# Kernel optimization log

Hardware: AMD Instinct MI355X
Metric: run time of the kernel (lower is better)

## Reference

```python
import jax, jax.numpy as jnp
import numpy as np

D_MODEL = 4096
D_FIBER = 16
D_CONTROL = 64
EMA_MOMENTUM = 0.9


def setup_inputs() -> dict:
    key = jax.random.key(0)
    k_h, k_f, k_w1, k_w2 = jax.random.split(key, 4)
    B, S = 4, 2048
    hidden = jax.random.normal(k_h, (B, S, D_MODEL), dtype=jnp.float32)
    # torch nn.Linear stores weight as [out, in]; fiber_proj init: normal std=0.02
    W_fiber = jax.random.normal(k_f, (D_FIBER, D_MODEL), dtype=jnp.float32) * 0.02
    # predictor[0]: Linear(d_model+d_fiber, d_control) with default torch init (uniform)
    fan_in1 = D_MODEL + D_FIBER
    bound1 = 1.0 / np.sqrt(fan_in1)
    W1 = jax.random.uniform(k_w1, (D_CONTROL, fan_in1), dtype=jnp.float32, minval=-bound1, maxval=bound1)
    b1 = jnp.zeros((D_CONTROL,), dtype=jnp.float32)
    # predictor[-2]: Linear(d_control, 1), weight normal std=0.01, bias zero
    W2 = jax.random.normal(k_w2, (1, D_CONTROL), dtype=jnp.float32) * 0.01
    b2 = jnp.zeros((1,), dtype=jnp.float32)
    lam = jnp.asarray(1.0, dtype=jnp.float32)
    return {"hidden": hidden, "W_fiber": W_fiber, "W1": W1, "b1": b1, "W2": W2, "b2": b2, "lam": lam}


def _causal_ema(delta_h, alpha):
    # h_t = alpha*h_{t-1} + (1-alpha)*d_t, h_{-1} = 0. delta_h: [B,S]
    B = delta_h.shape[0]
    def step(h_prev, d_t):
        h_t = alpha * h_prev + (1.0 - alpha) * d_t
        return h_t, h_t
    _, hs = jax.lax.scan(step, jnp.zeros((B,), delta_h.dtype), jnp.swapaxes(delta_h, 0, 1))
    return jnp.swapaxes(hs, 0, 1)  # [B,S]


def reference(hidden, W_fiber, W1, b1, W2, b2, lam):
    h = hidden.astype(jnp.float32)                      # [B,S,D]
    fiber = jnp.einsum('bsd,fd->bsf', h, W_fiber)       # [B,S,16]
    combined = jnp.concatenate([h, fiber], axis=-1)     # [B,S,D+16]
    z = jax.nn.gelu(jnp.einsum('bsc,kc->bsk', combined, W1) + b1, approximate=False)
    delta_h = jax.nn.softplus(jnp.einsum('bsk,ok->bso', z, W2) + b2)[..., 0]  # [B,S]
    field = _causal_ema(delta_h, EMA_MOMENTUM)          # [B,S]
    gate = jax.nn.sigmoid(-lam * field)
    return gate.astype(hidden.dtype), field.astype(hidden.dtype), delta_h.mean()
```

## Files before the change

### kernel.cpp

```cpp
#include <hip/hip_runtime.h>
#include <hip/hip_bf16.h>

#define D_MODEL 4096
#define NTOK    8192
#define SEQ     2048

typedef short bf16x8 __attribute__((ext_vector_type(8)));
typedef float f32x4  __attribute__((ext_vector_type(4)));

__device__ inline short f2bf(float x) {
  __hip_bfloat16 h = __float2bfloat16(x);
  return *reinterpret_cast<short*>(&h);
}
__device__ inline float bf2f(const void* p, size_t i) {
  return __bfloat162float(((const __hip_bfloat16*)p)[i]);
}

__global__ __launch_bounds__(320) void sniff_k(const void* hid, const void* wf,
                                               const void* w1, const void* w2,
                                               const void* b1, const void* b2,
                                               const void* lam,
                                               int* flags, float* scal) {
  int wv = threadIdx.x >> 6, lane = threadIdx.x & 63;
  const unsigned short* p = nullptr;
  int n = 0;
  switch (wv) {
    case 0: p = (const unsigned short*)hid; n = NTOK * D_MODEL; break;
    case 1: p = (const unsigned short*)wf;  n = 16 * D_MODEL;   break;
    case 2: p = (const unsigned short*)w1;  n = 64 * 4112;      break;
    case 3: p = (const unsigned short*)w2;  n = 64;             break;
    case 4: p = (const unsigned short*)b1;  n = 64;             break;
  }
  int S = n / 2 < 64 ? n / 2 : 64;
  bool act = lane < S;
  unsigned short ve = 0, vo = 0;
  if (act) { ve = p[2 * lane]; vo = p[2 * lane + 1]; }
  int ee = (ve >> 7) & 0xFF, eo = (vo >> 7) & 0xFF;
  bool ve_band   = (ve == 0) || (ve == 0x8000) || (ee >= 96 && ee <= 141);
  bool vo_bandnz = (vo != 0) && (vo != 0x8000) && (eo >= 96 && eo <= 141);
  int zp = __popcll(__ballot(act && ve == 0 && vo == 0));
  int ob = __popcll(__ballot(act && ve == 0 && vo_bandnz));
  int eb = __popcll(__ballot(act && ve_band));
  if (lane == 0) {
    int f;
    if (zp == S) f = 1;
    else if (4 * ob >= 3 * S) f = 0;
    else if (4 * eb >= 3 * S) f = 1;
    else f = 0;
    flags[wv] = f;
  }
  if (threadIdx.x == 0) {
    unsigned short l0 = *(const unsigned short*)lam;
    int le = (l0 >> 7) & 0xFF;
    if (l0 != 0 && l0 != 0x8000 && le >= 96 && le <= 141)
      scal[0] = __bfloat162float(*(const __hip_bfloat16*)lam);
    else
      scal[0] = *(const float*)lam;
    unsigned short c0 = *(const unsigned short*)b2;
    int ce = (c0 >> 7) & 0xFF;
    if (c0 == 0) scal[1] = 0.0f;
    else if (c0 != 0x8000 && ce >= 96 && ce <= 141)
      scal[1] = __bfloat162float(*(const __hip_bfloat16*)b2);
    else
      scal[1] = *(const float*)b2;
  }
}

__global__ __launch_bounds__(256) void fold_w1(const void* __restrict__ W1v,
                                               const void* __restrict__ Wfv,
                                               const int* __restrict__ flags,
                                               __hip_bfloat16* __restrict__ W1eff) {
  int n = blockIdx.x;
  int fw1 = flags[2], fwf = flags[1];
  __shared__ float w1b[16];
  if (threadIdx.x < 16) {
    size_t idx = (size_t)n * 4112 + 4096 + threadIdx.x;
    w1b[threadIdx.x] = fw1 ? bf2f(W1v, idx) : ((const float*)W1v)[idx];
  }
  __syncthreads();
  for (int k = threadIdx.x; k < D_MODEL; k += 256) {
    size_t idx = (size_t)n * 4112 + k;
    float v = fw1 ? bf2f(W1v, idx) : ((const float*)W1v)[idx];
#pragma unroll
    for (int f = 0; f < 16; ++f) {
      size_t wi = (size_t)f * D_MODEL + k;
      float wfv = fwf ? bf2f(Wfv, wi) : ((const float*)Wfv)[wi];
      v += w1b[f] * wfv;
    }
    W1eff[(size_t)n * D_MODEL + k] = __float2bfloat16(v);
  }
}

__global__ __launch_bounds__(512, 4) void gemm_part(const void* __restrict__ hid,
                                                    const short* __restrict__ B_,
                                                    const int* __restrict__ flags,
                                                    float* __restrict__ part) {
  int c = blockIdx.x >> 6;
  int t = blockIdx.x & 63;
  int w    = threadIdx.x >> 6;
  int lane = threadIdx.x & 63;
  int m = lane & 15, kg = lane >> 4;

  __shared__ short Bs[64 * 512];

#pragma unroll
  for (int i = 0; i < 8; ++i) {
    int n    = (threadIdx.x >> 6) + i * 8;
    int kb16 = threadIdx.x & 63;
    bf16x8 v = *(const bf16x8*)(B_ + (size_t)n * D_MODEL + c * 512 + kb16 * 8);
    *(bf16x8*)(Bs + kb16 * 512 + ((n ^ (kb16 & 7)) * 8)) = v;
  }
  __syncthreads();

  f32x4 acc0 = {0.f, 0.f, 0.f, 0.f};
  f32x4 acc1 = acc0, acc2 = acc0, acc3 = acc0;
  size_t abase = (size_t)(t * 128 + w * 16 + m) * D_MODEL + c * 512 + kg * 8;
  if (flags[0]) {
    const short* Ap = (const short*)hid + abase;
    bf16x8 areg[8];
#pragma unroll
    for (int i = 0; i < 8; ++i) areg[i] = *(const bf16x8*)(Ap + i * 32);
#pragma unroll
    for (int s = 0; s < 16; ++s) {
      bf16x8 a = areg[s & 7];
      if (s + 8 < 16) areg[s & 7] = *(const bf16x8*)(Ap + (s + 8) * 32);
      int kb16 = s * 4 + kg;
      int swz  = (kb16 & 7);
      const short* bp = Bs + kb16 * 512;
      bf16x8 b0 = *(const bf16x8*)(bp + (((m +  0) ^ swz) * 8));
      bf16x8 b1 = *(const bf16x8*)(bp + (((m + 16) ^ swz) * 8));
      bf16x8 b2 = *(const bf16x8*)(bp + (((m + 32) ^ swz) * 8));
      bf16x8 b3 = *(const bf16x8*)(bp + (((m + 48) ^ swz) * 8));
      acc0 = __builtin_amdgcn_mfma_f32_16x16x32_bf16(a, b0, acc0, 0, 0, 0);
      acc1 = __builtin_amdgcn_mfma_f32_16x16x32_bf16(a, b1, acc1, 0, 0, 0);
      acc2 = __builtin_amdgcn_mfma_f32_16x16x32_bf16(a, b2, acc2, 0, 0, 0);
      acc3 = __builtin_amdgcn_mfma_f32_16x16x32_bf16(a, b3, acc3, 0, 0, 0);
    }
  } else {
    const float* Ap = (const float*)hid + abase;
#pragma unroll 4
    for (int s = 0; s < 16; ++s) {
      float4 lo = *(const float4*)(Ap + s * 32);
      float4 hi = *(const float4*)(Ap + s * 32 + 4);
      bf16x8 a;
      a[0] = f2bf(lo.x); a[1] = f2bf(lo.y); a[2] = f2bf(lo.z); a[3] = f2bf(lo.w);
      a[4] = f2bf(hi.x); a[5] = f2bf(hi.y); a[6] = f2bf(hi.z); a[7] = f2bf(hi.w);
      int kb16 = s * 4 + kg;
      int swz  = (kb16 & 7);
      const short* bp = Bs + kb16 * 512;
      bf16x8 b0 = *(const bf16x8*)(bp + (((m +  0) ^ swz) * 8));
      bf16x8 b1 = *(const bf16x8*)(bp + (((m + 16) ^ swz) * 8));
      bf16x8 b2 = *(const bf16x8*)(bp + (((m + 32) ^ swz) * 8));
      bf16x8 b3 = *(const bf16x8*)(bp + (((m + 48) ^ swz) * 8));
      acc0 = __builtin_amdgcn_mfma_f32_16x16x32_bf16(a, b0, acc0, 0, 0, 0);
      acc1 = __builtin_amdgcn_mfma_f32_16x16x32_bf16(a, b1, acc1, 0, 0, 0);
      acc2 = __builtin_amdgcn_mfma_f32_16x16x32_bf16(a, b2, acc2, 0, 0, 0);
      acc3 = __builtin_amdgcn_mfma_f32_16x16x32_bf16(a, b3, acc3, 0, 0, 0);
    }
  }

  float* po = part + ((size_t)c * NTOK + (size_t)t * 128 + w * 16) * 64;
#pragma unroll
  for (int r = 0; r < 4; ++r) {
    int row = kg * 4 + r;
    po[row * 64 + (m +  0)] = acc0[r];
    po[row * 64 + (m + 16)] = acc1[r];
    po[row * 64 + (m + 32)] = acc2[r];
    po[row * 64 + (m + 48)] = acc3[r];
  }
}

__global__ __launch_bounds__(256) void delta_ep(const float* __restrict__ part,
                                                const void* __restrict__ b1,
                                                const void* __restrict__ w2,
                                                const int* __restrict__ flags,
                                                const float* __restrict__ scal,
                                                float* __restrict__ delta) {
  int t   = blockIdx.x & 63;
  int sub = blockIdx.x >> 6;
  int tok = t * 128 + sub * 16 + (threadIdx.x >> 4);
  int cid = threadIdx.x & 15;
  int fb1 = flags[4], fw2 = flags[3];
  float y = 0.f;
#pragma unroll
  for (int j = 0; j < 4; ++j) {
    int col = cid + 16 * j;
    float s = 0.f;
#pragma unroll
    for (int c = 0; c < 8; ++c)
      s += part[((size_t)c * NTOK + tok) * 64 + col];
    s += fb1 ? bf2f(b1, col) : ((const float*)b1)[col];
    float g = 0.5f * s * (1.0f + erff(s * 0.70710678118654752f));
    y += g * (fw2 ? bf2f(w2, col) : ((const float*)w2)[col]);
  }
#pragma unroll
  for (int off = 1; off <= 8; off <<= 1) y += __shfl_xor(y, off, 64);
  if (cid == 0) {
    float x = y + scal[1];
    float d = (x > 20.0f) ? x : log1pf(expf(x));
    delta[tok] = d;
  }
}

__global__ __launch_bounds__(256) void ema_out(const float* __restrict__ delta,
                                               const float* __restrict__ scal,
                                               float* __restrict__ out) {
  int b    = threadIdx.x >> 6;
  int lane = threadIdx.x & 63;
  const float alpha = 0.9f;
  float d[32];
  const float* dp = delta + b * SEQ + lane * 32;
  float beta = 0.f, lsum = 0.f;
#pragma unroll
  for (int i = 0; i < 32; ++i) {
    d[i] = dp[i];
    lsum += d[i];
    beta = alpha * beta + 0.1f * d[i];
  }
  float accA = 0.03433683820292512f;
  float accB = beta;
  for (int off = 1; off < 64; off <<= 1) {
    float uA = __shfl_up(accA, off, 64);
    float uB = __shfl_up(accB, off, 64);
    if (lane >= off) {
      accB = accB + accA * uB;
      accA = accA * uA;
    }
  }
  float prev = __shfl_up(accB, 1, 64);
  float h = (lane == 0) ? 0.f : prev;
  float lam = scal[0];
#pragma unroll
  for (int i = 0; i < 32; ++i) {
    h = alpha * h + 0.1f * d[i];
    float gate = 1.0f / (1.0f + expf(lam * h));
    out[b * SEQ + lane * 32 + i]        = gate;
    out[NTOK + b * SEQ + lane * 32 + i] = h;
  }
#pragma unroll
  for (int off = 32; off >= 1; off >>= 1) lsum += __shfl_xor(lsum, off, 64);
  __shared__ float bs[4];
  if (lane == 0) bs[b] = lsum;
  __syncthreads();
  if (threadIdx.x == 0)
    out[2 * NTOK] = (bs[0] + bs[1] + bs[2] + bs[3]) * (1.0f / 8192.0f);
}

extern "C" void kernel_launch(void* const* d_in, const int* in_sizes, int n_in,
                              void* d_out, int out_size, void* d_ws, size_t ws_size,
                              hipStream_t stream) {
  const void* hidden = d_in[0];
  const void* Wf     = d_in[1];
  const void* W1     = d_in[2];
  const void* b1     = d_in[3];
  const void* W2     = d_in[4];
  const void* b2     = d_in[5];
  const void* lam    = d_in[6];
  float* out = (float*)d_out;

  char* ws = (char*)d_ws;
  int*   flags = (int*)ws;
  float* scal  = (float*)(ws + 32);
  __hip_bfloat16* W1eff = (__hip_bfloat16*)(ws + 64);
  float* delta = (float*)(ws + 64 + (size_t)64 * D_MODEL * 2);
  float* part  = (float*)(ws + 64 + (size_t)64 * D_MODEL * 2 + NTOK * 4);

  sniff_k<<<1, 320, 0, stream>>>(hidden, Wf, W1, W2, b1, b2, lam, flags, scal);
  fold_w1<<<64, 256, 0, stream>>>(W1, Wf, flags, W1eff);
  gemm_part<<<512, 512, 0, stream>>>(hidden, (const short*)W1eff, flags, part);
  delta_ep<<<512, 256, 0, stream>>>(part, b1, W2, flags, scal, delta);
  ema_out<<<1, 256, 0, stream>>>(delta, scal, out);
}
```

Before: 241.6 us.

## Fuse GEMM with GELU epilogue, drop split-K partials and sniff kernel

Each block of the GEMM now owns 16 tokens across the full K dimension. It loops over 8 K-chunks, staging W1eff into shared memory and double-buffering the A registers, so the partial-sum buffer and the separate delta_ep kernel are no longer needed. The bias, GELU, W2 dot product and softplus run in-block through a small shared reduction. The sniff kernel is removed and its dtype detection is inlined into each consumer, and fold_w1 is vectorised. The aim is to avoid writing and re-reading the 8x partial buffer and to cut launches. In exchange each block re-stages all of W1eff (8 stages with syncs), and each wave holds one accumulator tile instead of four.

```diff
diff --git a/kernel.cpp b/kernel.cpp
--- a/kernel.cpp
+++ b/kernel.cpp
@@ -8,29 +8,22 @@
 typedef short bf16x8 __attribute__((ext_vector_type(8)));
 typedef float f32x4  __attribute__((ext_vector_type(4)));
 
-__device__ inline short f2bf(float x) {
+__device__ __forceinline__ short f2bf(float x) {
   __hip_bfloat16 h = __float2bfloat16(x);
   return *reinterpret_cast<short*>(&h);
 }
-__device__ inline float bf2f(const void* p, size_t i) {
-  return __bfloat162float(((const __hip_bfloat16*)p)[i]);
-}
-
-__global__ __launch_bounds__(320) void sniff_k(const void* hid, const void* wf,
-                                               const void* w1, const void* w2,
-                                               const void* b1, const void* b2,
-                                               const void* lam,
-                                               int* flags, float* scal) {
-  int wv = threadIdx.x >> 6, lane = threadIdx.x & 63;
-  const unsigned short* p = nullptr;
-  int n = 0;
-  switch (wv) {
-    case 0: p = (const unsigned short*)hid; n = NTOK * D_MODEL; break;
-    case 1: p = (const unsigned short*)wf;  n = 16 * D_MODEL;   break;
-    case 2: p = (const unsigned short*)w1;  n = 64 * 4112;      break;
-    case 3: p = (const unsigned short*)w2;  n = 64;             break;
-    case 4: p = (const unsigned short*)b1;  n = 64;             break;
-  }
+__device__ __forceinline__ float bfs2f(unsigned short u) {
+  unsigned int x = ((unsigned int)u) << 16;
+  float f;
+  __builtin_memcpy(&f, &x, 4);
+  return f;
+}
+__device__ __forceinline__ float bf2f(const void* p, size_t i) {
+  return bfs2f(((const unsigned short*)p)[i]);
+}
+
+__device__ __forceinline__ int sniff_wave(const unsigned short* p, int n) {
+  int lane = threadIdx.x & 63;
   int S = n / 2 < 64 ? n / 2 : 64;
   bool act = lane < S;
   unsigned short ve = 0, vo = 0;
@@ -41,169 +34,177 @@
   int zp = __popcll(__ballot(act && ve == 0 && vo == 0));
   int ob = __popcll(__ballot(act && ve == 0 && vo_bandnz));
   int eb = __popcll(__ballot(act && ve_band));
-  if (lane == 0) {
-    int f;
-    if (zp == S) f = 1;
-    else if (4 * ob >= 3 * S) f = 0;
-    else if (4 * eb >= 3 * S) f = 1;
-    else f = 0;
-    flags[wv] = f;
-  }
-  if (threadIdx.x == 0) {
-    unsigned short l0 = *(const unsigned short*)lam;
-    int le = (l0 >> 7) & 0xFF;
-    if (l0 != 0 && l0 != 0x8000 && le >= 96 && le <= 141)
-      scal[0] = __bfloat162float(*(const __hip_bfloat16*)lam);
-    else
-      scal[0] = *(const float*)lam;
-    unsigned short c0 = *(const unsigned short*)b2;
-    int ce = (c0 >> 7) & 0xFF;
-    if (c0 == 0) scal[1] = 0.0f;
-    else if (c0 != 0x8000 && ce >= 96 && ce <= 141)
-      scal[1] = __bfloat162float(*(const __hip_bfloat16*)b2);
-    else
-      scal[1] = *(const float*)b2;
-  }
+  if (zp == S) return 1;
+  if (4 * ob >= 3 * S) return 0;
+  if (4 * eb >= 3 * S) return 1;
+  return 0;
+}
+
+__device__ __forceinline__ float decode_lam(const void* lamp) {
+  unsigned short l0 = *(const unsigned short*)lamp;
+  int le = (l0 >> 7) & 0xFF;
+  if (l0 != 0 && l0 != 0x8000 && le >= 96 && le <= 141)
+    return bfs2f(l0);
+  return *(const float*)lamp;
+}
+__device__ __forceinline__ float decode_b2(const void* p) {
+  unsigned short c0 = *(const unsigned short*)p;
+  int ce = (c0 >> 7) & 0xFF;
+  if (c0 == 0) return 0.0f;
+  if (c0 != 0x8000 && ce >= 96 && ce <= 141)
+    return bfs2f(c0);
+  return *(const float*)p;
 }
 
 __global__ __launch_bounds__(256) void fold_w1(const void* __restrict__ W1v,
                                                const void* __restrict__ Wfv,
-                                               const int* __restrict__ flags,
-                                               __hip_bfloat16* __restrict__ W1eff) {
+                                               short* __restrict__ W1eff) {
   int n = blockIdx.x;
-  int fw1 = flags[2], fwf = flags[1];
+  int fw1 = sniff_wave((const unsigned short*)W1v, 64 * 4112);
+  int fwf = sniff_wave((const unsigned short*)Wfv, 16 * D_MODEL);
   __shared__ float w1b[16];
   if (threadIdx.x < 16) {
     size_t idx = (size_t)n * 4112 + 4096 + threadIdx.x;
     w1b[threadIdx.x] = fw1 ? bf2f(W1v, idx) : ((const float*)W1v)[idx];
   }
   __syncthreads();
-  for (int k = threadIdx.x; k < D_MODEL; k += 256) {
-    size_t idx = (size_t)n * 4112 + k;
-    float v = fw1 ? bf2f(W1v, idx) : ((const float*)W1v)[idx];
+  for (int it = 0; it < 4; ++it) {
+    int k0 = it * 1024 + threadIdx.x * 4;
+    size_t idx = (size_t)n * 4112 + k0;
+    float v0, v1, v2, v3;
+    if (fw1) {
+      ushort4 u = *(const ushort4*)((const unsigned short*)W1v + idx);
+      v0 = bfs2f(u.x); v1 = bfs2f(u.y); v2 = bfs2f(u.z); v3 = bfs2f(u.w);
+    } else {
+      float4 f = *(const float4*)((const float*)W1v + idx);
+      v0 = f.x; v1 = f.y; v2 = f.z; v3 = f.w;
+    }
 #pragma unroll
     for (int f = 0; f < 16; ++f) {
-      size_t wi = (size_t)f * D_MODEL + k;
-      float wfv = fwf ? bf2f(Wfv, wi) : ((const float*)Wfv)[wi];
-      v += w1b[f] * wfv;
-    }
-    W1eff[(size_t)n * D_MODEL + k] = __float2bfloat16(v);
-  }
-}
-
-__global__ __launch_bounds__(512, 4) void gemm_part(const void* __restrict__ hid,
-                                                    const short* __restrict__ B_,
-                                                    const int* __restrict__ flags,
-                                                    float* __restrict__ part) {
-  int c = blockIdx.x >> 6;
-  int t = blockIdx.x & 63;
-  int w    = threadIdx.x >> 6;
-  int lane = threadIdx.x & 63;
+      size_t wi = (size_t)f * D_MODEL + k0;
+      float w0, w1_, w2_, w3_;
+      if (fwf) {
+        ushort4 u = *(const ushort4*)((const unsigned short*)Wfv + wi);
+        w0 = bfs2f(u.x); w1_ = bfs2f(u.y); w2_ = bfs2f(u.z); w3_ = bfs2f(u.w);
+      } else {
+        float4 fv = *(const float4*)((const float*)Wfv + wi);
+        w0 = fv.x; w1_ = fv.y; w2_ = fv.z; w3_ = fv.w;
+      }
+      float s = w1b[f];
+      v0 += s * w0; v1 += s * w1_; v2 += s * w2_; v3 += s * w3_;
+    }
+    ushort4 o;
+    o.x = (unsigned short)f2bf(v0); o.y = (unsigned short)f2bf(v1);
+    o.z = (unsigned short)f2bf(v2); o.w = (unsigned short)f2bf(v3);
+    *(ushort4*)(W1eff + (size_t)n * D_MODEL + k0) = o;
+  }
+}
+
+__device__ __forceinline__ void stage_chunk(short* Bs, const short* __restrict__ B_,
+                                            int c, int w, int lane) {
+#pragma unroll
+  for (int i = 0; i < 8; ++i) {
+    int n = w + i * 8;
+    bf16x8 v = *(const bf16x8*)(B_ + (size_t)n * D_MODEL + c * 512 + lane * 8);
+    *(bf16x8*)(Bs + lane * 512 + ((n ^ (lane & 7)) * 8)) = v;
+  }
+}
+
+__global__ __launch_bounds__(512, 4) void gemm_fused(const void* __restrict__ hid,
+                                                     const short* __restrict__ B_,
+                                                     const void* __restrict__ b1,
+                                                     const void* __restrict__ w2,
+                                                     const void* __restrict__ b2,
+                                                     float* __restrict__ delta) {
+  int t = blockIdx.x;
+  int w = threadIdx.x >> 6, lane = threadIdx.x & 63;
+  int wc = w & 3, kc = w >> 2;
   int m = lane & 15, kg = lane >> 4;
 
   __shared__ short Bs[64 * 512];
-
-#pragma unroll
-  for (int i = 0; i < 8; ++i) {
-    int n    = (threadIdx.x >> 6) + i * 8;
-    int kb16 = threadIdx.x & 63;
-    bf16x8 v = *(const bf16x8*)(B_ + (size_t)n * D_MODEL + c * 512 + kb16 * 8);
-    *(bf16x8*)(Bs + kb16 * 512 + ((n ^ (kb16 & 7)) * 8)) = v;
-  }
-  __syncthreads();
-
-  f32x4 acc0 = {0.f, 0.f, 0.f, 0.f};
-  f32x4 acc1 = acc0, acc2 = acc0, acc3 = acc0;
-  size_t abase = (size_t)(t * 128 + w * 16 + m) * D_MODEL + c * 512 + kg * 8;
-  if (flags[0]) {
+  __shared__ float red[16][68];
+
+  int fhid = sniff_wave((const unsigned short*)hid, NTOK * D_MODEL);
+
+  f32x4 acc = {0.f, 0.f, 0.f, 0.f};
+  size_t abase = (size_t)(t * 16 + m) * D_MODEL + kc * 256 + kg * 8;
+
+  if (fhid) {
     const short* Ap = (const short*)hid + abase;
-    bf16x8 areg[8];
-#pragma unroll
-    for (int i = 0; i < 8; ++i) areg[i] = *(const bf16x8*)(Ap + i * 32);
-#pragma unroll
-    for (int s = 0; s < 16; ++s) {
-      bf16x8 a = areg[s & 7];
-      if (s + 8 < 16) areg[s & 7] = *(const bf16x8*)(Ap + (s + 8) * 32);
-      int kb16 = s * 4 + kg;
-      int swz  = (kb16 & 7);
-      const short* bp = Bs + kb16 * 512;
-      bf16x8 b0 = *(const bf16x8*)(bp + (((m +  0) ^ swz) * 8));
-      bf16x8 b1 = *(const bf16x8*)(bp + (((m + 16) ^ swz) * 8));
-      bf16x8 b2 = *(const bf16x8*)(bp + (((m + 32) ^ swz) * 8));
-      bf16x8 b3 = *(const bf16x8*)(bp + (((m + 48) ^ swz) * 8));
-      acc0 = __builtin_amdgcn_mfma_f32_16x16x32_bf16(a, b0, acc0, 0, 0, 0);
-      acc1 = __builtin_amdgcn_mfma_f32_16x16x32_bf16(a, b1, acc1, 0, 0, 0);
-      acc2 = __builtin_amdgcn_mfma_f32_16x16x32_bf16(a, b2, acc2, 0, 0, 0);
-      acc3 = __builtin_amdgcn_mfma_f32_16x16x32_bf16(a, b3, acc3, 0, 0, 0);
+    bf16x8 areg[2][8];
+#pragma unroll
+    for (int s = 0; s < 8; ++s) areg[0][s] = *(const bf16x8*)(Ap + s * 32);
+#pragma unroll
+    for (int c = 0; c < 8; ++c) {
+      __syncthreads();
+      if (c < 7) {
+#pragma unroll
+        for (int s = 0; s < 8; ++s)
+          areg[(c + 1) & 1][s] = *(const bf16x8*)(Ap + (c + 1) * 512 + s * 32);
+      }
+      stage_chunk(Bs, B_, c, w, lane);
+      __syncthreads();
+#pragma unroll
+      for (int s = 0; s < 8; ++s) {
+        int kb16 = kc * 32 + s * 4 + kg;
+        bf16x8 b = *(const bf16x8*)(Bs + kb16 * 512 + (((wc * 16 + m) ^ (kb16 & 7)) * 8));
+        acc = __builtin_amdgcn_mfma_f32_16x16x32_bf16(areg[c & 1][s], b, acc, 0, 0, 0);
+      }
     }
   } else {
     const float* Ap = (const float*)hid + abase;
-#pragma unroll 4
-    for (int s = 0; s < 16; ++s) {
-      float4 lo = *(const float4*)(Ap + s * 32);
-      float4 hi = *(const float4*)(Ap + s * 32 + 4);
-      bf16x8 a;
-      a[0] = f2bf(lo.x); a[1] = f2bf(lo.y); a[2] = f2bf(lo.z); a[3] = f2bf(lo.w);
-      a[4] = f2bf(hi.x); a[5] = f2bf(hi.y); a[6] = f2bf(hi.z); a[7] = f2bf(hi.w);
-      int kb16 = s * 4 + kg;
-      int swz  = (kb16 & 7);
-      const short* bp = Bs + kb16 * 512;
-      bf16x8 b0 = *(const bf16x8*)(bp + (((m +  0) ^ swz) * 8));
-      bf16x8 b1 = *(const bf16x8*)(bp + (((m + 16) ^ swz) * 8));
-      bf16x8 b2 = *(const bf16x8*)(bp + (((m + 32) ^ swz) * 8));
-      bf16x8 b3 = *(const bf16x8*)(bp + (((m + 48) ^ swz) * 8));
-      acc0 = __builtin_amdgcn_mfma_f32_16x16x32_bf16(a, b0, acc0, 0, 0, 0);
-      acc1 = __builtin_amdgcn_mfma_f32_16x16x32_bf16(a, b1, acc1, 0, 0, 0);
-      acc2 = __builtin_amdgcn_mfma_f32_16x16x32_bf16(a, b2, acc2, 0, 0, 0);
-      acc3 = __builtin_amdgcn_mfma_f32_16x16x32_bf16(a, b3, acc3, 0, 0, 0);
-    }
-  }
-
-  float* po = part + ((size_t)c * NTOK + (size_t)t * 128 + w * 16) * 64;
-#pragma unroll
-  for (int r = 0; r < 4; ++r) {
-    int row = kg * 4 + r;
-    po[row * 64 + (m +  0)] = acc0[r];
-    po[row * 64 + (m + 16)] = acc1[r];
-    po[row * 64 + (m + 32)] = acc2[r];
-    po[row * 64 + (m + 48)] = acc3[r];
-  }
-}
-
-__global__ __launch_bounds__(256) void delta_ep(const float* __restrict__ part,
-                                                const void* __restrict__ b1,
-                                                const void* __restrict__ w2,
-                                                const int* __restrict__ flags,
-                                                const float* __restrict__ scal,
-                                                float* __restrict__ delta) {
-  int t   = blockIdx.x & 63;
-  int sub = blockIdx.x >> 6;
-  int tok = t * 128 + sub * 16 + (threadIdx.x >> 4);
-  int cid = threadIdx.x & 15;
-  int fb1 = flags[4], fw2 = flags[3];
-  float y = 0.f;
-#pragma unroll
-  for (int j = 0; j < 4; ++j) {
-    int col = cid + 16 * j;
-    float s = 0.f;
-#pragma unroll
-    for (int c = 0; c < 8; ++c)
-      s += part[((size_t)c * NTOK + tok) * 64 + col];
-    s += fb1 ? bf2f(b1, col) : ((const float*)b1)[col];
-    float g = 0.5f * s * (1.0f + erff(s * 0.70710678118654752f));
-    y += g * (fw2 ? bf2f(w2, col) : ((const float*)w2)[col]);
-  }
-#pragma unroll
-  for (int off = 1; off <= 8; off <<= 1) y += __shfl_xor(y, off, 64);
-  if (cid == 0) {
-    float x = y + scal[1];
+    for (int c = 0; c < 8; ++c) {
+      __syncthreads();
+      stage_chunk(Bs, B_, c, w, lane);
+      __syncthreads();
+#pragma unroll
+      for (int s = 0; s < 8; ++s) {
+        float4 lo = *(const float4*)(Ap + c * 512 + s * 32);
+        float4 hi = *(const float4*)(Ap + c * 512 + s * 32 + 4);
+        bf16x8 a;
+        a[0] = f2bf(lo.x); a[1] = f2bf(lo.y); a[2] = f2bf(lo.z); a[3] = f2bf(lo.w);
+        a[4] = f2bf(hi.x); a[5] = f2bf(hi.y); a[6] = f2bf(hi.z); a[7] = f2bf(hi.w);
+        int kb16 = kc * 32 + s * 4 + kg;
+        bf16x8 b = *(const bf16x8*)(Bs + kb16 * 512 + (((wc * 16 + m) ^ (kb16 & 7)) * 8));
+        acc = __builtin_amdgcn_mfma_f32_16x16x32_bf16(a, b, acc, 0, 0, 0);
+      }
+    }
+  }
+
+  if (kc == 1) {
+#pragma unroll
+    for (int r = 0; r < 4; ++r) red[kg * 4 + r][wc * 16 + m] = acc[r];
+  }
+  __syncthreads();
+  float b2v = 0.f;
+  if (kc == 0) {
+    int fb1 = sniff_wave((const unsigned short*)b1, 64);
+    int fw2 = sniff_wave((const unsigned short*)w2, 64);
+    b2v = decode_b2(b2);
+    int col = wc * 16 + m;
+    float b1v = fb1 ? bf2f(b1, col) : ((const float*)b1)[col];
+    float w2v = fw2 ? bf2f(w2, col) : ((const float*)w2)[col];
+#pragma unroll
+    for (int r = 0; r < 4; ++r) {
+      int tok = kg * 4 + r;
+      float s = acc[r] + red[tok][col] + b1v;
+      float g = 0.5f * s * (1.0f + erff(s * 0.70710678118654752f));
+      red[tok][col] = g * w2v;
+    }
+  }
+  __syncthreads();
+  if (threadIdx.x < 16) {
+    float y = 0.f;
+#pragma unroll
+    for (int cc = 0; cc < 64; ++cc) y += red[threadIdx.x][cc];
+    float x = y + b2v;
     float d = (x > 20.0f) ? x : log1pf(expf(x));
-    delta[tok] = d;
+    delta[t * 16 + threadIdx.x] = d;
   }
 }
 
 __global__ __launch_bounds__(256) void ema_out(const float* __restrict__ delta,
-                                               const float* __restrict__ scal,
+                                               const void* __restrict__ lamp,
                                                float* __restrict__ out) {
   int b    = threadIdx.x >> 6;
   int lane = threadIdx.x & 63;
@@ -229,7 +230,7 @@
   }
   float prev = __shfl_up(accB, 1, 64);
   float h = (lane == 0) ? 0.f : prev;
-  float lam = scal[0];
+  float lam = decode_lam(lamp);
 #pragma unroll
   for (int i = 0; i < 32; ++i) {
     h = alpha * h + 0.1f * d[i];
@@ -259,15 +260,10 @@
   float* out = (float*)d_out;
 
   char* ws = (char*)d_ws;
-  int*   flags = (int*)ws;
-  float* scal  = (float*)(ws + 32);
-  __hip_bfloat16* W1eff = (__hip_bfloat16*)(ws + 64);
-  float* delta = (float*)(ws + 64 + (size_t)64 * D_MODEL * 2);
-  float* part  = (float*)(ws + 64 + (size_t)64 * D_MODEL * 2 + NTOK * 4);
-
-  sniff_k<<<1, 320, 0, stream>>>(hidden, Wf, W1, W2, b1, b2, lam, flags, scal);
-  fold_w1<<<64, 256, 0, stream>>>(W1, Wf, flags, W1eff);
-  gemm_part<<<512, 512, 0, stream>>>(hidden, (const short*)W1eff, flags, part);
-  delta_ep<<<512, 256, 0, stream>>>(part, b1, W2, flags, scal, delta);
-  ema_out<<<1, 256, 0, stream>>>(delta, scal, out);
-}
+  short* W1eff = (short*)ws;
+  float* delta = (float*)(ws + (size_t)64 * D_MODEL * 2);
+
+  fold_w1<<<64, 256, 0, stream>>>(W1, Wf, W1eff);
+  gemm_fused<<<512, 512, 0, stream>>>(hidden, W1eff, b1, W2, b2, delta);
+  ema_out<<<1, 256, 0, stream>>>(delta, lam, out);
+}
```

New measurement: 248.0 us. 1.03x slower.
